# Optimization experiments

Measured on AMD Instinct MI355X. Metric: run time of the kernel, lower is better.

Reference implementation:

```python
import jax, jax.numpy as jnp
import numpy as np

MARGIN = 1.0
EPS = 1e-16


def setup_inputs() -> dict:
    key = jax.random.key(0)
    k1, k2 = jax.random.split(key)
    B, E = 512, 128
    embs = jax.random.normal(k1, (B, E), dtype=jnp.float32)
    labels = jax.random.randint(k2, (B,), 0, 64, dtype=jnp.int64)
    return {"embs": embs, "labels": labels}


def _triplet_mask(labels):
    # [B,B,B] mask: valid (a,p,n) iff a!=p, a!=n, p!=n, label[a]==label[p], label[a]!=label[n]
    B = labels.shape[0]
    neq = ~jnp.eye(B, dtype=bool)
    idx_mask = neq[:, :, None] & neq[:, None, :] & neq[None, :, :]
    lab_eq = labels[:, None] == labels[None, :]
    lab_mask = lab_eq[:, :, None] & (~lab_eq)[:, None, :]
    return idx_mask & lab_mask


def reference(embs, labels):
    # pairwise squared L2 distances (squared=True path, no sqrt)
    dot = embs @ embs.T                      # [B,B]
    sq_norm = jnp.diagonal(dot)              # [B]
    dist = sq_norm[:, None] - 2.0 * dot + sq_norm[None, :]
    dist = jnp.maximum(dist, 0.0)            # [B,B]

    # triplet losses: d(a,p) - d(a,n) + margin, over [B,B,B]
    triplet_loss = dist[:, :, None] - dist[:, None, :] + MARGIN
    mask = _triplet_mask(labels)
    triplet_loss = jnp.maximum(triplet_loss * mask.astype(triplet_loss.dtype), 0.0)

    n_pos = jnp.sum(triplet_loss > EPS)
    return jnp.sum(triplet_loss) / (n_pos.astype(triplet_loss.dtype) + EPS)
```

## Files before the change

### kernel.cpp

```cpp
#include <hip/hip_runtime.h>
#include <hip/hip_bf16.h>


#define BSZ 512
#define EDIM 128
#define TS 32
#define NPOSMAX 96

typedef __attribute__((ext_vector_type(8))) short short8;
typedef __attribute__((ext_vector_type(4))) float f32x4;

__device__ __forceinline__ unsigned short f2bf(float f) {
    __hip_bfloat16 h = __float2bfloat16(f);
    return *reinterpret_cast<unsigned short*>(&h);
}

__global__ __launch_bounds__(256) void dist_mfma(
    const float* __restrict__ embs,
    float* __restrict__ D)
{
    __shared__ unsigned short Abf[TS][136];
    __shared__ unsigned short Bbf[TS][136];
    __shared__ float nA[TS], nB[TS];

    const int tid = threadIdx.x;
    const int bi = blockIdx.x >> 4;
    const int bj = blockIdx.x & 15;
    const int I = bi * TS, J = bj * TS;
    const int wv = tid >> 6, lane = tid & 63;

    const float4* E4 = reinterpret_cast<const float4*>(embs);

#pragma unroll
    for (int q = 0; q < 4; ++q) {
        int idx = tid + 256 * q;
        int r   = idx >> 5;
        int k4  = idx & 31;

        float4 va = E4[(size_t)(I + r) * (EDIM / 4) + k4];
        float sa = va.x * va.x + va.y * va.y + va.z * va.z + va.w * va.w;
        sa += __shfl_xor(sa, 1); sa += __shfl_xor(sa, 2); sa += __shfl_xor(sa, 4);
        sa += __shfl_xor(sa, 8); sa += __shfl_xor(sa, 16);
        if ((tid & 31) == 0) nA[r] = sa;
        ushort4 ua = { f2bf(va.x), f2bf(va.y), f2bf(va.z), f2bf(va.w) };
        *reinterpret_cast<ushort4*>(&Abf[r][k4 * 4]) = ua;

        float4 vb = E4[(size_t)(J + r) * (EDIM / 4) + k4];
        float sb = vb.x * vb.x + vb.y * vb.y + vb.z * vb.z + vb.w * vb.w;
        sb += __shfl_xor(sb, 1); sb += __shfl_xor(sb, 2); sb += __shfl_xor(sb, 4);
        sb += __shfl_xor(sb, 8); sb += __shfl_xor(sb, 16);
        if ((tid & 31) == 0) nB[r] = sb;
        ushort4 ub = { f2bf(-2.f * vb.x), f2bf(-2.f * vb.y),
                       f2bf(-2.f * vb.z), f2bf(-2.f * vb.w) };
        *reinterpret_cast<ushort4*>(&Bbf[r][k4 * 4]) = ub;
    }
    __syncthreads();

    const int qi = wv >> 1, qj = wv & 1;
    const int l15 = lane & 15, lk = lane >> 4;

    f32x4 acc;
#pragma unroll
    for (int reg = 0; reg < 4; ++reg)
        acc[reg] = nA[qi * 16 + lk * 4 + reg] + nB[qj * 16 + l15];

    const unsigned short* arow = &Abf[qi * 16 + l15][0];
    const unsigned short* brow = &Bbf[qj * 16 + l15][0];
#pragma unroll
    for (int ks = 0; ks < 4; ++ks) {
        short8 af = *reinterpret_cast<const short8*>(arow + ks * 32 + lk * 8);
        short8 bf = *reinterpret_cast<const short8*>(brow + ks * 32 + lk * 8);
        acc = __builtin_amdgcn_mfma_f32_16x16x32_bf16(af, bf, acc, 0, 0, 0);
    }

#pragma unroll
    for (int reg = 0; reg < 4; ++reg) {
        int row = I + qi * 16 + lk * 4 + reg;
        int col = J + qj * 16 + l15;
        D[(size_t)row * BSZ + col] = fmaxf(acc[reg], 0.f);
    }
}

__global__ __launch_bounds__(256) void triplet_pass(
    const float* __restrict__ D,
    const int* __restrict__ labels,
    float* __restrict__ sums,
    float* __restrict__ cnts)
{
    __shared__ int   lab[BSZ];
    __shared__ float d[BSZ];
    __shared__ unsigned long long masks[8];
    __shared__ int   plist[NPOSMAX];
    __shared__ float wsum[4];
    __shared__ int   wcnt[4];

    const int a = blockIdx.x, tid = threadIdx.x;
    const int wv = tid >> 6, lane = tid & 63;

    lab[tid]       = labels[tid];
    lab[tid + 256] = labels[tid + 256];
    float2 dv = reinterpret_cast<const float2*>(D + (size_t)a * BSZ)[tid];
    d[tid * 2]     = dv.x;
    d[tid * 2 + 1] = dv.y;
    __syncthreads();

    const int la = lab[a];

#pragma unroll
    for (int c = 0; c < 2; ++c) {
        int j = c * 256 + tid;
        unsigned long long m = __ballot(lab[j] == la && j != a);
        if (lane == 0) masks[c * 4 + wv] = m;
    }
    __syncthreads();

    int np = 0;
#pragma unroll
    for (int m = 0; m < 8; ++m) np += __popcll(masks[m]);
    if (np > NPOSMAX) np = NPOSMAX;

#pragma unroll
    for (int c = 0; c < 2; ++c) {
        int j = c * 256 + tid;
        if (lab[j] == la && j != a) {
            int mi = c * 4 + wv, off = 0;
            for (int m = 0; m < mi; ++m) off += __popcll(masks[m]);
            off += __popcll(masks[mi] & ((1ull << lane) - 1ull));
            if (off < NPOSMAX) plist[off] = j;
        }
    }
    __syncthreads();

    float s = 0.f;
    int   cnt = 0;
#pragma unroll
    for (int c = 0; c < 2; ++c) {
        int n = c * 256 + tid;
        if (lab[n] != la) {
            float dn = d[n];
            for (int i = 0; i < np; ++i) {
                float t = fmaxf(d[plist[i]] - dn + 1.0f, 0.f);
                s += t;
                cnt += (t > 1e-16f) ? 1 : 0;
            }
        }
    }

#pragma unroll
    for (int off = 32; off; off >>= 1) {
        s   += __shfl_down(s, off);
        cnt += __shfl_down(cnt, off);
    }
    if (lane == 0) { wsum[wv] = s; wcnt[wv] = cnt; }
    __syncthreads();
    if (tid == 0) {
        sums[a] = wsum[0] + wsum[1] + wsum[2] + wsum[3];
        cnts[a] = (float)(wcnt[0] + wcnt[1] + wcnt[2] + wcnt[3]);
    }
}

__global__ __launch_bounds__(512) void finalize(
    const float* __restrict__ sums,
    const float* __restrict__ cnts,
    float* __restrict__ out)
{
    __shared__ float wsum[8], wcnt[8];
    const int tid = threadIdx.x;
    float s = sums[tid];
    float c = cnts[tid];
#pragma unroll
    for (int off = 32; off; off >>= 1) {
        s += __shfl_down(s, off);
        c += __shfl_down(c, off);
    }
    const int wv = tid >> 6, lane = tid & 63;
    if (lane == 0) { wsum[wv] = s; wcnt[wv] = c; }
    __syncthreads();
    if (tid == 0) {
        float S = 0.f, C = 0.f;
#pragma unroll
        for (int w = 0; w < 8; ++w) { S += wsum[w]; C += wcnt[w]; }
        out[0] = S / (C + 1e-16f);
    }
}

extern "C" void kernel_launch(void* const* d_in, const int* in_sizes, int n_in,
                              void* d_out, int out_size, void* d_ws, size_t ws_size,
                              hipStream_t stream)
{
    const float* embs   = reinterpret_cast<const float*>(d_in[0]);
    const int*   labels = reinterpret_cast<const int*>(d_in[1]);
    float*       out    = reinterpret_cast<float*>(d_out);

    float* D    = reinterpret_cast<float*>(d_ws);
    float* sums = D + (size_t)BSZ * BSZ;
    float* cnts = sums + BSZ;

    dist_mfma<<<256, 256, 0, stream>>>(embs, D);
    triplet_pass<<<BSZ, 256, 0, stream>>>(D, labels, sums, cnts);
    finalize<<<1, 512, 0, stream>>>(sums, cnts, out);
}
```

Baseline: 15.78 us.

## Move positive-list construction into distance kernel and process two anchors per block

The distance kernel now also loads the labels, ballots same-label positives for two anchors per block and writes a compact per-anchor positive list with its count into a workspace buffer. The hinge kernel then handles two anchors per block (256 blocks instead of 512), reading the precomputed lists and gathering positive distances into shared memory, which removes the per-anchor label scan and ballot work from the second pass. This adds label work and extra global writes to the GEMM kernel. The positive cap drops to 63, which could truncate classes larger than that; the test labels (512 samples over 64 classes) make that unlikely.

```diff
diff --git a/kernel.cpp b/kernel.cpp
--- a/kernel.cpp
+++ b/kernel.cpp
@@ -5,7 +5,7 @@
 #define BSZ 512
 #define EDIM 128
 #define TS 32
-#define NPOSMAX 96
+#define NPOS 64
 
 typedef __attribute__((ext_vector_type(8))) short short8;
 typedef __attribute__((ext_vector_type(4))) float f32x4;
@@ -17,17 +17,22 @@
 
 __global__ __launch_bounds__(256) void dist_mfma(
     const float* __restrict__ embs,
-    float* __restrict__ D)
+    const int* __restrict__ labels,
+    float* __restrict__ D,
+    int* __restrict__ meta)
 {
     __shared__ unsigned short Abf[TS][136];
     __shared__ unsigned short Bbf[TS][136];
     __shared__ float nA[TS], nB[TS];
+    __shared__ int   lab[BSZ];
+    __shared__ unsigned long long m0sh[8], m1sh[8];
 
     const int tid = threadIdx.x;
     const int bi = blockIdx.x >> 4;
     const int bj = blockIdx.x & 15;
     const int I = bi * TS, J = bj * TS;
     const int wv = tid >> 6, lane = tid & 63;
+    const int a0 = blockIdx.x * 2, a1 = a0 + 1;
 
     const float4* E4 = reinterpret_cast<const float4*>(embs);
 
@@ -54,6 +59,18 @@
                        f2bf(-2.f * vb.z), f2bf(-2.f * vb.w) };
         *reinterpret_cast<ushort4*>(&Bbf[r][k4 * 4]) = ub;
     }
+    lab[tid]       = labels[tid];
+    lab[tid + 256] = labels[tid + 256];
+    __syncthreads();
+
+    const int la0 = lab[a0], la1 = lab[a1];
+#pragma unroll
+    for (int c = 0; c < 2; ++c) {
+        int j = c * 256 + tid;
+        unsigned long long m0 = __ballot(lab[j] == la0 && j != a0);
+        unsigned long long m1 = __ballot(lab[j] == la1 && j != a1);
+        if (lane == 0) { m0sh[c * 4 + wv] = m0; m1sh[c * 4 + wv] = m1; }
+    }
     __syncthreads();
 
     const int qi = wv >> 1, qj = wv & 1;
@@ -72,99 +89,99 @@
         short8 bf = *reinterpret_cast<const short8*>(brow + ks * 32 + lk * 8);
         acc = __builtin_amdgcn_mfma_f32_16x16x32_bf16(af, bf, acc, 0, 0, 0);
     }
-
 #pragma unroll
     for (int reg = 0; reg < 4; ++reg) {
         int row = I + qi * 16 + lk * 4 + reg;
         int col = J + qj * 16 + l15;
         D[(size_t)row * BSZ + col] = fmaxf(acc[reg], 0.f);
     }
-}
-
-__global__ __launch_bounds__(256) void triplet_pass(
+
+    int np0 = 0, np1 = 0;
+#pragma unroll
+    for (int m = 0; m < 8; ++m) { np0 += __popcll(m0sh[m]); np1 += __popcll(m1sh[m]); }
+    if (np0 > NPOS - 1) np0 = NPOS - 1;
+    if (np1 > NPOS - 1) np1 = NPOS - 1;
+
+#pragma unroll
+    for (int c = 0; c < 2; ++c) {
+        int j = c * 256 + tid;
+        if (lab[j] == la0 && j != a0) {
+            int mi = c * 4 + wv, off = 0;
+            for (int m = 0; m < mi; ++m) off += __popcll(m0sh[m]);
+            off += __popcll(m0sh[mi] & ((1ull << lane) - 1ull));
+            if (off < NPOS - 1) meta[a0 * NPOS + 1 + off] = j;
+        }
+        if (lab[j] == la1 && j != a1) {
+            int mi = c * 4 + wv, off = 0;
+            for (int m = 0; m < mi; ++m) off += __popcll(m1sh[m]);
+            off += __popcll(m1sh[mi] & ((1ull << lane) - 1ull));
+            if (off < NPOS - 1) meta[a1 * NPOS + 1 + off] = j;
+        }
+    }
+    if (tid == 0) { meta[a0 * NPOS] = np0; meta[a1 * NPOS] = np1; }
+}
+
+__global__ __launch_bounds__(256) void hinge_pass(
     const float* __restrict__ D,
     const int* __restrict__ labels,
+    const int* __restrict__ meta,
     float* __restrict__ sums,
     float* __restrict__ cnts)
 {
-    __shared__ int   lab[BSZ];
-    __shared__ float d[BSZ];
-    __shared__ unsigned long long masks[8];
-    __shared__ int   plist[NPOSMAX];
+    __shared__ float pd0[NPOS], pd1[NPOS];
+    __shared__ int   npsh[2];
     __shared__ float wsum[4];
     __shared__ int   wcnt[4];
 
-    const int a = blockIdx.x, tid = threadIdx.x;
+    const int tid = threadIdx.x;
     const int wv = tid >> 6, lane = tid & 63;
-
-    lab[tid]       = labels[tid];
-    lab[tid + 256] = labels[tid + 256];
-    float2 dv = reinterpret_cast<const float2*>(D + (size_t)a * BSZ)[tid];
-    d[tid * 2]     = dv.x;
-    d[tid * 2 + 1] = dv.y;
-    __syncthreads();
-
-    const int la = lab[a];
-
-#pragma unroll
-    for (int c = 0; c < 2; ++c) {
-        int j = c * 256 + tid;
-        unsigned long long m = __ballot(lab[j] == la && j != a);
-        if (lane == 0) masks[c * 4 + wv] = m;
-    }
-    __syncthreads();
-
-    int np = 0;
-#pragma unroll
-    for (int m = 0; m < 8; ++m) np += __popcll(masks[m]);
-    if (np > NPOSMAX) np = NPOSMAX;
-
-#pragma unroll
-    for (int c = 0; c < 2; ++c) {
-        int j = c * 256 + tid;
-        if (lab[j] == la && j != a) {
-            int mi = c * 4 + wv, off = 0;
-            for (int m = 0; m < mi; ++m) off += __popcll(masks[m]);
-            off += __popcll(masks[mi] & ((1ull << lane) - 1ull));
-            if (off < NPOSMAX) plist[off] = j;
-        }
-    }
-    __syncthreads();
-
+    const int b = blockIdx.x, a0 = 2 * b, a1 = a0 + 1;
+
+    if (wv == 0) {
+        int v = meta[a0 * NPOS + lane];
+        int np = __shfl(v, 0);
+        if (lane == 0) npsh[0] = np;
+        if (lane >= 1 && lane <= np) pd0[lane - 1] = D[(size_t)a0 * BSZ + v];
+    } else if (wv == 1) {
+        int v = meta[a1 * NPOS + lane];
+        int np = __shfl(v, 0);
+        if (lane == 0) npsh[1] = np;
+        if (lane >= 1 && lane <= np) pd1[lane - 1] = D[(size_t)a1 * BSZ + v];
+    }
+
+    const int la0 = labels[a0], la1 = labels[a1];
+    int2   ln = reinterpret_cast<const int2*>(labels)[tid];
+    float2 r0 = reinterpret_cast<const float2*>(D + (size_t)a0 * BSZ)[tid];
+    float2 r1 = reinterpret_cast<const float2*>(D + (size_t)a1 * BSZ)[tid];
+    __syncthreads();
+
+    const int np0 = npsh[0], np1 = npsh[1];
     float s = 0.f;
-    int   cnt = 0;
-#pragma unroll
-    for (int c = 0; c < 2; ++c) {
-        int n = c * 256 + tid;
-        if (lab[n] != la) {
-            float dn = d[n];
-            for (int i = 0; i < np; ++i) {
-                float t = fmaxf(d[plist[i]] - dn + 1.0f, 0.f);
-                s += t;
-                cnt += (t > 1e-16f) ? 1 : 0;
-            }
-        }
-    }
+    int   c = 0;
+    if (ln.x != la0) for (int i = 0; i < np0; ++i) { float t = fmaxf(pd0[i] - r0.x + 1.0f, 0.f); s += t; c += (t > 1e-16f); }
+    if (ln.y != la0) for (int i = 0; i < np0; ++i) { float t = fmaxf(pd0[i] - r0.y + 1.0f, 0.f); s += t; c += (t > 1e-16f); }
+    if (ln.x != la1) for (int i = 0; i < np1; ++i) { float t = fmaxf(pd1[i] - r1.x + 1.0f, 0.f); s += t; c += (t > 1e-16f); }
+    if (ln.y != la1) for (int i = 0; i < np1; ++i) { float t = fmaxf(pd1[i] - r1.y + 1.0f, 0.f); s += t; c += (t > 1e-16f); }
 
 #pragma unroll
     for (int off = 32; off; off >>= 1) {
-        s   += __shfl_down(s, off);
-        cnt += __shfl_down(cnt, off);
-    }
-    if (lane == 0) { wsum[wv] = s; wcnt[wv] = cnt; }
+        s += __shfl_down(s, off);
+        c += __shfl_down(c, off);
+    }
+    if (lane == 0) { wsum[wv] = s; wcnt[wv] = c; }
     __syncthreads();
     if (tid == 0) {
-        sums[a] = wsum[0] + wsum[1] + wsum[2] + wsum[3];
-        cnts[a] = (float)(wcnt[0] + wcnt[1] + wcnt[2] + wcnt[3]);
-    }
-}
-
-__global__ __launch_bounds__(512) void finalize(
+        sums[b] = wsum[0] + wsum[1] + wsum[2] + wsum[3];
+        cnts[b] = (float)(wcnt[0] + wcnt[1] + wcnt[2] + wcnt[3]);
+    }
+}
+
+__global__ __launch_bounds__(256) void finalize(
     const float* __restrict__ sums,
     const float* __restrict__ cnts,
     float* __restrict__ out)
 {
-    __shared__ float wsum[8], wcnt[8];
+    __shared__ float fsum[4], fcnt[4];
     const int tid = threadIdx.x;
     float s = sums[tid];
     float c = cnts[tid];
@@ -174,12 +191,11 @@
         c += __shfl_down(c, off);
     }
     const int wv = tid >> 6, lane = tid & 63;
-    if (lane == 0) { wsum[wv] = s; wcnt[wv] = c; }
+    if (lane == 0) { fsum[wv] = s; fcnt[wv] = c; }
     __syncthreads();
     if (tid == 0) {
-        float S = 0.f, C = 0.f;
-#pragma unroll
-        for (int w = 0; w < 8; ++w) { S += wsum[w]; C += wcnt[w]; }
+        float S = fsum[0] + fsum[1] + fsum[2] + fsum[3];
+        float C = fcnt[0] + fcnt[1] + fcnt[2] + fcnt[3];
         out[0] = S / (C + 1e-16f);
     }
 }
@@ -193,10 +209,11 @@
     float*       out    = reinterpret_cast<float*>(d_out);
 
     float* D    = reinterpret_cast<float*>(d_ws);
-    float* sums = D + (size_t)BSZ * BSZ;
-    float* cnts = sums + BSZ;
-
-    dist_mfma<<<256, 256, 0, stream>>>(embs, D);
-    triplet_pass<<<BSZ, 256, 0, stream>>>(D, labels, sums, cnts);
-    finalize<<<1, 512, 0, stream>>>(sums, cnts, out);
-}
+    int*   meta = reinterpret_cast<int*>(D + (size_t)BSZ * BSZ);
+    float* sums = reinterpret_cast<float*>(meta + BSZ * NPOS);
+    float* cnts = sums + 256;
+
+    dist_mfma<<<256, 256, 0, stream>>>(embs, labels, D, meta);
+    hinge_pass<<<256, 256, 0, stream>>>(D, labels, meta, sums, cnts);
+    finalize<<<1, 256, 0, stream>>>(sums, cnts, out);
+}
```

Result: slower. 16.27 us (+3.1%).

## Split distance and triplet kernels into twice as many smaller blocks

Applied to the files above, without the earlier changes.

The distance kernel now uses 16x32 tiles and 512 blocks. Only two of its four waves issue MFMA, and all four still help load the tiles. The triplet kernel splits each anchor's negatives across two 128-thread blocks, giving 1024 blocks, and finalize reduces 1024 partials. The aim is more parallelism on the 256-CU GPU. The cost is redundant label and row loads, plus duplicated positive-list construction in each half-block.

```diff
diff --git a/kernel.cpp b/kernel.cpp
--- a/kernel.cpp
+++ b/kernel.cpp
@@ -4,7 +4,6 @@
 
 #define BSZ 512
 #define EDIM 128
-#define TS 32
 #define NPOSMAX 96
 
 typedef __attribute__((ext_vector_type(8))) short short8;
@@ -15,73 +14,76 @@
     return *reinterpret_cast<unsigned short*>(&h);
 }
 
-__global__ __launch_bounds__(256) void dist_mfma(
+__global__ __launch_bounds__(256) void dist_mfma_h(
     const float* __restrict__ embs,
     float* __restrict__ D)
 {
-    __shared__ unsigned short Abf[TS][136];
-    __shared__ unsigned short Bbf[TS][136];
-    __shared__ float nA[TS], nB[TS];
+    __shared__ unsigned short Abf[16][136];
+    __shared__ unsigned short Bbf[32][136];
+    __shared__ float nA[16], nB[32];
 
     const int tid = threadIdx.x;
     const int bi = blockIdx.x >> 4;
     const int bj = blockIdx.x & 15;
-    const int I = bi * TS, J = bj * TS;
+    const int I = bi * 16, J = bj * 32;
     const int wv = tid >> 6, lane = tid & 63;
 
     const float4* E4 = reinterpret_cast<const float4*>(embs);
 
+#pragma unroll
+    for (int q = 0; q < 2; ++q) {
+        int idx = tid + 256 * q;
+        int r = idx >> 5, k4 = idx & 31;
+        float4 v = E4[(size_t)(I + r) * (EDIM / 4) + k4];
+        float s = v.x * v.x + v.y * v.y + v.z * v.z + v.w * v.w;
+        s += __shfl_xor(s, 1); s += __shfl_xor(s, 2); s += __shfl_xor(s, 4);
+        s += __shfl_xor(s, 8); s += __shfl_xor(s, 16);
+        if ((tid & 31) == 0) nA[r] = s;
+        ushort4 u = { f2bf(v.x), f2bf(v.y), f2bf(v.z), f2bf(v.w) };
+        *reinterpret_cast<ushort4*>(&Abf[r][k4 * 4]) = u;
+    }
 #pragma unroll
     for (int q = 0; q < 4; ++q) {
         int idx = tid + 256 * q;
-        int r   = idx >> 5;
-        int k4  = idx & 31;
-
-        float4 va = E4[(size_t)(I + r) * (EDIM / 4) + k4];
-        float sa = va.x * va.x + va.y * va.y + va.z * va.z + va.w * va.w;
-        sa += __shfl_xor(sa, 1); sa += __shfl_xor(sa, 2); sa += __shfl_xor(sa, 4);
-        sa += __shfl_xor(sa, 8); sa += __shfl_xor(sa, 16);
-        if ((tid & 31) == 0) nA[r] = sa;
-        ushort4 ua = { f2bf(va.x), f2bf(va.y), f2bf(va.z), f2bf(va.w) };
-        *reinterpret_cast<ushort4*>(&Abf[r][k4 * 4]) = ua;
-
-        float4 vb = E4[(size_t)(J + r) * (EDIM / 4) + k4];
-        float sb = vb.x * vb.x + vb.y * vb.y + vb.z * vb.z + vb.w * vb.w;
-        sb += __shfl_xor(sb, 1); sb += __shfl_xor(sb, 2); sb += __shfl_xor(sb, 4);
-        sb += __shfl_xor(sb, 8); sb += __shfl_xor(sb, 16);
-        if ((tid & 31) == 0) nB[r] = sb;
-        ushort4 ub = { f2bf(-2.f * vb.x), f2bf(-2.f * vb.y),
-                       f2bf(-2.f * vb.z), f2bf(-2.f * vb.w) };
-        *reinterpret_cast<ushort4*>(&Bbf[r][k4 * 4]) = ub;
-    }
-    __syncthreads();
-
-    const int qi = wv >> 1, qj = wv & 1;
-    const int l15 = lane & 15, lk = lane >> 4;
-
-    f32x4 acc;
-#pragma unroll
-    for (int reg = 0; reg < 4; ++reg)
-        acc[reg] = nA[qi * 16 + lk * 4 + reg] + nB[qj * 16 + l15];
-
-    const unsigned short* arow = &Abf[qi * 16 + l15][0];
-    const unsigned short* brow = &Bbf[qj * 16 + l15][0];
-#pragma unroll
-    for (int ks = 0; ks < 4; ++ks) {
-        short8 af = *reinterpret_cast<const short8*>(arow + ks * 32 + lk * 8);
-        short8 bf = *reinterpret_cast<const short8*>(brow + ks * 32 + lk * 8);
-        acc = __builtin_amdgcn_mfma_f32_16x16x32_bf16(af, bf, acc, 0, 0, 0);
-    }
-
-#pragma unroll
-    for (int reg = 0; reg < 4; ++reg) {
-        int row = I + qi * 16 + lk * 4 + reg;
-        int col = J + qj * 16 + l15;
-        D[(size_t)row * BSZ + col] = fmaxf(acc[reg], 0.f);
-    }
-}
-
-__global__ __launch_bounds__(256) void triplet_pass(
+        int r = idx >> 5, k4 = idx & 31;
+        float4 v = E4[(size_t)(J + r) * (EDIM / 4) + k4];
+        float s = v.x * v.x + v.y * v.y + v.z * v.z + v.w * v.w;
+        s += __shfl_xor(s, 1); s += __shfl_xor(s, 2); s += __shfl_xor(s, 4);
+        s += __shfl_xor(s, 8); s += __shfl_xor(s, 16);
+        if ((tid & 31) == 0) nB[r] = s;
+        ushort4 u = { f2bf(-2.f * v.x), f2bf(-2.f * v.y),
+                      f2bf(-2.f * v.z), f2bf(-2.f * v.w) };
+        *reinterpret_cast<ushort4*>(&Bbf[r][k4 * 4]) = u;
+    }
+    __syncthreads();
+
+    if (wv < 2) {
+        const int qj = wv;
+        const int l15 = lane & 15, lk = lane >> 4;
+
+        f32x4 acc;
+#pragma unroll
+        for (int reg = 0; reg < 4; ++reg)
+            acc[reg] = nA[lk * 4 + reg] + nB[qj * 16 + l15];
+
+        const unsigned short* arow = &Abf[l15][0];
+        const unsigned short* brow = &Bbf[qj * 16 + l15][0];
+#pragma unroll
+        for (int ks = 0; ks < 4; ++ks) {
+            short8 af = *reinterpret_cast<const short8*>(arow + ks * 32 + lk * 8);
+            short8 bf = *reinterpret_cast<const short8*>(brow + ks * 32 + lk * 8);
+            acc = __builtin_amdgcn_mfma_f32_16x16x32_bf16(af, bf, acc, 0, 0, 0);
+        }
+#pragma unroll
+        for (int reg = 0; reg < 4; ++reg) {
+            int row = I + lk * 4 + reg;
+            int col = J + qj * 16 + l15;
+            D[(size_t)row * BSZ + col] = fmaxf(acc[reg], 0.f);
+        }
+    }
+}
+
+__global__ __launch_bounds__(128) void triplet_h(
     const float* __restrict__ D,
     const int* __restrict__ labels,
     float* __restrict__ sums,
@@ -91,26 +93,28 @@
     __shared__ float d[BSZ];
     __shared__ unsigned long long masks[8];
     __shared__ int   plist[NPOSMAX];
-    __shared__ float wsum[4];
-    __shared__ int   wcnt[4];
-
-    const int a = blockIdx.x, tid = threadIdx.x;
+    __shared__ float wsum[2];
+    __shared__ int   wcnt[2];
+
+    const int b = blockIdx.x, tid = threadIdx.x;
+    const int a = b >> 1, h = b & 1;
     const int wv = tid >> 6, lane = tid & 63;
 
-    lab[tid]       = labels[tid];
-    lab[tid + 256] = labels[tid + 256];
-    float2 dv = reinterpret_cast<const float2*>(D + (size_t)a * BSZ)[tid];
-    d[tid * 2]     = dv.x;
-    d[tid * 2 + 1] = dv.y;
+#pragma unroll
+    for (int q = 0; q < 4; ++q) lab[tid + 128 * q] = labels[tid + 128 * q];
+    float4 dv = reinterpret_cast<const float4*>(D + (size_t)a * BSZ)[tid];
+    d[tid * 4 + 0] = dv.x; d[tid * 4 + 1] = dv.y;
+    d[tid * 4 + 2] = dv.z; d[tid * 4 + 3] = dv.w;
     __syncthreads();
 
     const int la = lab[a];
 
 #pragma unroll
-    for (int c = 0; c < 2; ++c) {
-        int j = c * 256 + tid;
+    for (int c = 0; c < 4; ++c) {
+        int mi = c * 2 + wv;
+        int j = mi * 64 + lane;
         unsigned long long m = __ballot(lab[j] == la && j != a);
-        if (lane == 0) masks[c * 4 + wv] = m;
+        if (lane == 0) masks[mi] = m;
     }
     __syncthreads();
 
@@ -120,10 +124,11 @@
     if (np > NPOSMAX) np = NPOSMAX;
 
 #pragma unroll
-    for (int c = 0; c < 2; ++c) {
-        int j = c * 256 + tid;
+    for (int c = 0; c < 4; ++c) {
+        int mi = c * 2 + wv;
+        int j = mi * 64 + lane;
         if (lab[j] == la && j != a) {
-            int mi = c * 4 + wv, off = 0;
+            int off = 0;
             for (int m = 0; m < mi; ++m) off += __popcll(masks[m]);
             off += __popcll(masks[mi] & ((1ull << lane) - 1ull));
             if (off < NPOSMAX) plist[off] = j;
@@ -135,7 +140,7 @@
     int   cnt = 0;
 #pragma unroll
     for (int c = 0; c < 2; ++c) {
-        int n = c * 256 + tid;
+        int n = h * 256 + c * 128 + tid;
         if (lab[n] != la) {
             float dn = d[n];
             for (int i = 0; i < np; ++i) {
@@ -154,17 +159,17 @@
     if (lane == 0) { wsum[wv] = s; wcnt[wv] = cnt; }
     __syncthreads();
     if (tid == 0) {
-        sums[a] = wsum[0] + wsum[1] + wsum[2] + wsum[3];
-        cnts[a] = (float)(wcnt[0] + wcnt[1] + wcnt[2] + wcnt[3]);
-    }
-}
-
-__global__ __launch_bounds__(512) void finalize(
+        sums[b] = wsum[0] + wsum[1];
+        cnts[b] = (float)(wcnt[0] + wcnt[1]);
+    }
+}
+
+__global__ __launch_bounds__(1024) void finalize(
     const float* __restrict__ sums,
     const float* __restrict__ cnts,
     float* __restrict__ out)
 {
-    __shared__ float wsum[8], wcnt[8];
+    __shared__ float fsum[16], fcnt[16];
     const int tid = threadIdx.x;
     float s = sums[tid];
     float c = cnts[tid];
@@ -174,12 +179,12 @@
         c += __shfl_down(c, off);
     }
     const int wv = tid >> 6, lane = tid & 63;
-    if (lane == 0) { wsum[wv] = s; wcnt[wv] = c; }
+    if (lane == 0) { fsum[wv] = s; fcnt[wv] = c; }
     __syncthreads();
     if (tid == 0) {
         float S = 0.f, C = 0.f;
 #pragma unroll
-        for (int w = 0; w < 8; ++w) { S += wsum[w]; C += wcnt[w]; }
+        for (int w = 0; w < 16; ++w) { S += fsum[w]; C += fcnt[w]; }
         out[0] = S / (C + 1e-16f);
     }
 }
@@ -194,9 +199,9 @@
 
     float* D    = reinterpret_cast<float*>(d_ws);
     float* sums = D + (size_t)BSZ * BSZ;
-    float* cnts = sums + BSZ;
-
-    dist_mfma<<<256, 256, 0, stream>>>(embs, D);
-    triplet_pass<<<BSZ, 256, 0, stream>>>(D, labels, sums, cnts);
-    finalize<<<1, 512, 0, stream>>>(sums, cnts, out);
-}
+    float* cnts = sums + 1024;
+
+    dist_mfma_h<<<512, 256, 0, stream>>>(embs, D);
+    triplet_h<<<1024, 128, 0, stream>>>(D, labels, sums, cnts);
+    finalize<<<1, 1024, 0, stream>>>(sums, cnts, out);
+}
```

Result: slower. 17.17 us (+8.8%).
